# Optimization experiments

Measured on AMD Instinct MI355X. Metric: run time of the kernel, lower is better.

Reference implementation:

```python
import jax, jax.numpy as jnp
import numpy as np

B, S, E, H = 8, 2048, 1024, 64

def setup_inputs() -> dict:
    key = jax.random.key(0)
    k1, k2, k3, k4 = jax.random.split(key, 4)
    scale = 0.02
    return {
        "x": jax.random.normal(k1, (B, S, E), dtype=jnp.float32),
        "Wq": jax.random.normal(k2, (E, H), dtype=jnp.float32) * scale,
        "Wk": jax.random.normal(k3, (E, H), dtype=jnp.float32) * scale,
        "Wv": jax.random.normal(k4, (E, H), dtype=jnp.float32) * scale,
    }

def reference(x, Wq, Wk, Wv):
    # x: [B, S, E]; projections to [B, S, H]
    q = jnp.einsum("bse,eh->bsh", x, Wq)
    k = jnp.einsum("bse,eh->bsh", x, Wk)
    v = jnp.einsum("bse,eh->bsh", x, Wv)
    head_size = Wq.shape[1]
    # NOTE: original divides by head_size (not sqrt(head_size))
    scores = jnp.einsum("bqh,bkh->bqk", q, k) / head_size  # [B, S, S]
    seq = q.shape[1]
    causal = jnp.tril(jnp.ones((seq, seq), dtype=bool))
    scores = jnp.where(causal, scores, -jnp.inf)
    attn = jax.nn.softmax(scores, axis=-1)
    # dropout p=0.0 (eval) -> identity
    return jnp.einsum("bqk,bkh->bqh", attn, v)
```

## Files before the change

kernel.cpp:

```cpp
#include <hip/hip_runtime.h>


typedef __bf16 bf16;
typedef bf16 bf16x8 __attribute__((ext_vector_type(8)));
typedef bf16 bf16x4 __attribute__((ext_vector_type(4)));
typedef float v4f __attribute__((ext_vector_type(4)));

#define MFMA_BF16 __builtin_amdgcn_mfma_f32_16x16x32_bf16

constexpr int SEQ = 2048, EDIM = 1024, HDIM = 64;
constexpr float SCALE_L2E = 1.4426950408889634f / 64.0f;

__global__ __launch_bounds__(256) void prep_w_kernel(
    const float* __restrict__ Wq, const float* __restrict__ Wk,
    const float* __restrict__ Wv, bf16* __restrict__ Wt) {
  int mat = blockIdx.x >> 5, kseg = blockIdx.x & 31;
  const float* src = mat == 0 ? Wq : (mat == 1 ? Wk : Wv);
  int n = threadIdx.x & 63;
  int k0 = kseg * 32 + (threadIdx.x >> 6) * 8;
  bf16x8 v;
#pragma unroll
  for (int j = 0; j < 8; ++j)
    v[j] = (bf16)src[(k0 + j) * 64 + n];
  *reinterpret_cast<bf16x8*>(Wt + (size_t)(mat * 64 + n) * EDIM + k0) = v;
}

__global__ __launch_bounds__(256) void proj_kernel(
    const float* __restrict__ x, const bf16* __restrict__ Wt,
    bf16* __restrict__ qw, bf16* __restrict__ kw, bf16* __restrict__ vT) {
  __shared__ __align__(16) bf16 As[2][32][72];
  __shared__ __align__(16) bf16 Bs[2][192][72];

  const int t = threadIdx.x;
  const int m0 = blockIdx.x * 32;
  const int wv = t >> 6, lane = t & 63, quad = lane >> 4, l16 = lane & 15;

  v4f acc[2][3] = {};
  float4 aReg[2];
  bf16x8 bReg[6];

  auto loadA = [&](int kk) {
#pragma unroll
    for (int p = 0; p < 2; ++p) {
      int flat = p * 1024 + t * 4;
      int r = flat >> 6, c = flat & 63;
      aReg[p] = *reinterpret_cast<const float4*>(
          x + (size_t)(m0 + r) * EDIM + kk * 64 + c);
    }
  };
  auto loadB = [&](int kk) {
#pragma unroll
    for (int p = 0; p < 6; ++p) {
      int idx = p * 256 + t;
      int r = idx >> 3, off = (idx & 7) * 8;
      bReg[p] = *reinterpret_cast<const bf16x8*>(
          Wt + (size_t)r * EDIM + kk * 64 + off);
    }
  };

  loadA(0);
  loadB(0);

  for (int kk = 0; kk < 16; ++kk) {
    const int buf = kk & 1;
#pragma unroll
    for (int p = 0; p < 2; ++p) {
      int flat = p * 1024 + t * 4;
      int r = flat >> 6, c = flat & 63;
      bf16x4 h4 = {(bf16)aReg[p].x, (bf16)aReg[p].y,
                   (bf16)aReg[p].z, (bf16)aReg[p].w};
      *reinterpret_cast<bf16x4*>(&As[buf][r][c]) = h4;
    }
#pragma unroll
    for (int p = 0; p < 6; ++p) {
      int idx = p * 256 + t;
      int r = idx >> 3, off = (idx & 7) * 8;
      *reinterpret_cast<bf16x8*>(&Bs[buf][r][off]) = bReg[p];
    }
    __syncthreads();
    if (kk < 15) {
      loadA(kk + 1);
      loadB(kk + 1);
    }
#pragma unroll
    for (int ks = 0; ks < 2; ++ks) {
      bf16x8 af[2], bfr[3];
#pragma unroll
      for (int mi = 0; mi < 2; ++mi)
        af[mi] = *reinterpret_cast<const bf16x8*>(
            &As[buf][16 * mi + l16][32 * ks + 8 * quad]);
#pragma unroll
      for (int ni = 0; ni < 3; ++ni)
        bfr[ni] = *reinterpret_cast<const bf16x8*>(
            &Bs[buf][48 * wv + 16 * ni + l16][32 * ks + 8 * quad]);
#pragma unroll
      for (int mi = 0; mi < 2; ++mi)
#pragma unroll
        for (int ni = 0; ni < 3; ++ni)
          acc[mi][ni] = MFMA_BF16(af[mi], bfr[ni], acc[mi][ni], 0, 0, 0);
    }
  }

#pragma unroll
  for (int mi = 0; mi < 2; ++mi) {
    const int token0 = m0 + 16 * mi + 4 * quad;
#pragma unroll
    for (int ni = 0; ni < 3; ++ni) {
      int n = 48 * wv + 16 * ni + l16;
      if (n < 64) {
#pragma unroll
        for (int r = 0; r < 4; ++r)
          qw[(size_t)(token0 + r) * HDIM + n] = (bf16)acc[mi][ni][r];
      } else if (n < 128) {
#pragma unroll
        for (int r = 0; r < 4; ++r)
          kw[(size_t)(token0 + r) * HDIM + (n - 64)] = (bf16)acc[mi][ni][r];
      } else {
        int b = token0 >> 11, s0 = token0 & 2047;
        bf16x4 pk = {(bf16)acc[mi][ni][0], (bf16)acc[mi][ni][1],
                     (bf16)acc[mi][ni][2], (bf16)acc[mi][ni][3]};
        *reinterpret_cast<bf16x4*>(
            vT + ((size_t)(b * 64 + (n - 128))) * SEQ + s0) = pk;
      }
    }
  }
}

__global__ __launch_bounds__(512) void attn_kernel(
    const bf16* __restrict__ qw, const bf16* __restrict__ kw,
    const bf16* __restrict__ vT, float* __restrict__ out) {
  const int batch = blockIdx.x & 7;
  const int pi = blockIdx.x >> 3;
  const int w = threadIdx.x >> 6;
  const int lane = threadIdx.x & 63;
  const int quad = lane >> 4, l16 = lane & 15;

  __shared__ __align__(16) bf16 p_lds[8][2][32][68];
  __shared__ __align__(16) float o_lds[8][32][68];
  __shared__ float l_lds[8][32];

  const bf16* qB = qw + (size_t)batch * SEQ * HDIM;
  const bf16* kB = kw + (size_t)batch * SEQ * HDIM;
  const bf16* vB = vT + (size_t)batch * HDIM * SEQ;

  for (int sp = 0; sp < 2; ++sp) {
    const int j = sp ? (63 - pi) : pi;
    const int q0 = 32 * j;
    const int T64 = (j + 2) >> 1;
    const int nw = (T64 > w) ? (((T64 - 1 - w) >> 3) + 1) : 0;

    bf16x8 aq[2][2];
#pragma unroll
    for (int mi = 0; mi < 2; ++mi)
#pragma unroll
      for (int kf = 0; kf < 2; ++kf)
        aq[mi][kf] = *reinterpret_cast<const bf16x8*>(
            qB + (size_t)(q0 + 16 * mi + l16) * HDIM + 32 * kf + 8 * quad);

    v4f accO[2][4] = {};
    float l_part[2][4] = {{0.f, 0.f, 0.f, 0.f}, {0.f, 0.f, 0.f, 0.f}};
    bf16x8 kfr[4][2];

    auto loadK = [&](int jt) {
#pragma unroll
      for (int nt = 0; nt < 4; ++nt)
#pragma unroll
        for (int kf = 0; kf < 2; ++kf)
          kfr[nt][kf] = *reinterpret_cast<const bf16x8*>(
              kB + (size_t)(64 * jt + 16 * nt + l16) * HDIM + 32 * kf +
              8 * quad);
    };
    auto qk_exp_stage = [&](int jt, int slot) {
      v4f s[2][4] = {};
#pragma unroll
      for (int mi = 0; mi < 2; ++mi)
#pragma unroll
        for (int nt = 0; nt < 4; ++nt) {
          s[mi][nt] = MFMA_BF16(aq[mi][0], kfr[nt][0], s[mi][nt], 0, 0, 0);
          s[mi][nt] = MFMA_BF16(aq[mi][1], kfr[nt][1], s[mi][nt], 0, 0, 0);
        }
      const bool last = (jt == T64 - 1);
#pragma unroll
      for (int mi = 0; mi < 2; ++mi)
#pragma unroll
        for (int nt = 0; nt < 4; ++nt)
#pragma unroll
          for (int r = 0; r < 4; ++r) {
            float p = __builtin_amdgcn_exp2f(s[mi][nt][r] * SCALE_L2E);
            if (last &&
                (64 * jt + 16 * nt + l16 > q0 + 16 * mi + 4 * quad + r))
              p = 0.f;
            l_part[mi][r] += p;
            p_lds[w][slot][16 * mi + 4 * quad + r][16 * nt + l16] = (bf16)p;
          }
    };

    if (nw > 0) {
      loadK(w);
      qk_exp_stage(w, 0);
    }
    for (int i = 0; i < nw; ++i) {
      const int jt = w + 8 * i;
      const int k0 = 64 * jt;
      if (i + 1 < nw) loadK(jt + 8);
      bf16x8 vfr[4][2];
#pragma unroll
      for (int nt = 0; nt < 4; ++nt)
#pragma unroll
        for (int kc = 0; kc < 2; ++kc)
          vfr[nt][kc] = *reinterpret_cast<const bf16x8*>(
              vB + (size_t)(16 * nt + l16) * SEQ + k0 + 32 * kc + 8 * quad);
      asm volatile("s_waitcnt lgkmcnt(0)" ::: "memory");
      bf16x8 pa[2][2];
#pragma unroll
      for (int mi = 0; mi < 2; ++mi)
#pragma unroll
        for (int kc = 0; kc < 2; ++kc)
          pa[mi][kc] = *reinterpret_cast<const bf16x8*>(
              &p_lds[w][i & 1][16 * mi + l16][32 * kc + 8 * quad]);
      if (i + 1 < nw) qk_exp_stage(jt + 8, (i + 1) & 1);
#pragma unroll
      for (int mi = 0; mi < 2; ++mi)
#pragma unroll
        for (int nt = 0; nt < 4; ++nt) {
          accO[mi][nt] = MFMA_BF16(pa[mi][0], vfr[nt][0], accO[mi][nt], 0, 0, 0);
          accO[mi][nt] = MFMA_BF16(pa[mi][1], vfr[nt][1], accO[mi][nt], 0, 0, 0);
        }
    }

#pragma unroll
    for (int mi = 0; mi < 2; ++mi)
#pragma unroll
      for (int r = 0; r < 4; ++r) {
        float s = l_part[mi][r];
        s += __shfl_xor(s, 1, 16);
        s += __shfl_xor(s, 2, 16);
        s += __shfl_xor(s, 4, 16);
        s += __shfl_xor(s, 8, 16);
        l_part[mi][r] = s;
      }

    __syncthreads();
#pragma unroll
    for (int mi = 0; mi < 2; ++mi)
#pragma unroll
      for (int nt = 0; nt < 4; ++nt)
#pragma unroll
        for (int r = 0; r < 4; ++r)
          o_lds[w][16 * mi + 4 * quad + r][16 * nt + l16] = accO[mi][nt][r];
    if (l16 == 0) {
#pragma unroll
      for (int mi = 0; mi < 2; ++mi)
#pragma unroll
        for (int r = 0; r < 4; ++r)
          l_lds[w][16 * mi + 4 * quad + r] = l_part[mi][r];
    }
    __syncthreads();

    {
      const int col = threadIdx.x & 63;
      const int r0 = (threadIdx.x >> 6) * 4;
#pragma unroll
      for (int k = 0; k < 4; ++k) {
        const int row = r0 + k;
        float lt = 0.f, s = 0.f;
#pragma unroll
        for (int c = 0; c < 8; ++c) {
          lt += l_lds[c][row];
          s += o_lds[c][row][col];
        }
        out[((size_t)batch * SEQ + q0 + row) * HDIM + col] = s / lt;
      }
    }
  }
}

extern "C" void kernel_launch(void* const* d_in, const int* in_sizes, int n_in,
                              void* d_out, int out_size, void* d_ws,
                              size_t ws_size, hipStream_t stream) {
  const float* x = (const float*)d_in[0];
  const float* Wq = (const float*)d_in[1];
  const float* Wk = (const float*)d_in[2];
  const float* Wv = (const float*)d_in[3];

  char* ws = (char*)d_ws;
  bf16* Wt = (bf16*)(ws);
  bf16* qw = (bf16*)(ws + 0x60000);
  bf16* kw = (bf16*)(ws + 0x260000);
  bf16* vT = (bf16*)(ws + 0x460000);

  prep_w_kernel<<<96, 256, 0, stream>>>(Wq, Wk, Wv, Wt);
  proj_kernel<<<512, 256, 0, stream>>>(x, Wt, qw, kw, vT);
  attn_kernel<<<256, 512, 0, stream>>>(qw, kw, vT, (float*)d_out);
}
```

Measured before the change: 136.7 us.

## Fuse weight prep, projection and attention into one cooperative kernel

```diff
diff --git a/kernel.cpp b/kernel.cpp
--- a/kernel.cpp
+++ b/kernel.cpp
@@ -1,4 +1,7 @@
 #include <hip/hip_runtime.h>
+#include <hip/hip_cooperative_groups.h>
+
+namespace cg = cooperative_groups;
 
 
 typedef __bf16 bf16;
@@ -10,6 +13,286 @@
 
 constexpr int SEQ = 2048, EDIM = 1024, HDIM = 64;
 constexpr float SCALE_L2E = 1.4426950408889634f / 64.0f;
+
+__global__ __launch_bounds__(512, 2) void fused_kernel(
+    const float* __restrict__ x, const float* __restrict__ Wq,
+    const float* __restrict__ Wk, const float* __restrict__ Wv,
+    bf16* __restrict__ Wt, bf16* __restrict__ qw, bf16* __restrict__ kw,
+    bf16* __restrict__ vT, float* __restrict__ out) {
+  __shared__ __align__(16) char smem[140288];
+  const int t = threadIdx.x;
+  const int lane = t & 63;
+  const int quad = lane >> 4, l16 = lane & 15;
+
+  {
+    const int gid = blockIdx.x * 512 + t;
+    if (gid < 24576) {
+      const int n = gid & 63;
+      const int k0 = ((gid >> 6) & 127) * 8;
+      const int mat = gid >> 13;
+      const float* src = mat == 0 ? Wq : (mat == 1 ? Wk : Wv);
+      bf16x8 v;
+#pragma unroll
+      for (int j = 0; j < 8; ++j)
+        v[j] = (bf16)src[(k0 + j) * 64 + n];
+      *reinterpret_cast<bf16x8*>(Wt + (size_t)(mat * 64 + n) * EDIM + k0) = v;
+    }
+  }
+  cg::this_grid().sync();
+
+  {
+    typedef bf16 AsArr[2][64][72];
+    typedef bf16 BsArr[2][192][72];
+    AsArr& As = *reinterpret_cast<AsArr*>(smem);
+    BsArr& Bs = *reinterpret_cast<BsArr*>(smem + sizeof(AsArr));
+
+    const int m0 = blockIdx.x * 64;
+    const int w8 = t >> 6;
+    const int wm = w8 >> 2;
+    const int wn = w8 & 3;
+
+    v4f acc[2][3] = {};
+    float4 aReg[2];
+    bf16x8 bReg[3];
+
+    auto loadA = [&](int kk) {
+#pragma unroll
+      for (int p = 0; p < 2; ++p) {
+        int flat = p * 2048 + t * 4;
+        int r = flat >> 6, c = flat & 63;
+        aReg[p] = *reinterpret_cast<const float4*>(
+            x + (size_t)(m0 + r) * EDIM + kk * 64 + c);
+      }
+    };
+    auto loadB = [&](int kk) {
+#pragma unroll
+      for (int p = 0; p < 3; ++p) {
+        int idx = p * 512 + t;
+        int r = idx >> 3, off = (idx & 7) * 8;
+        bReg[p] = *reinterpret_cast<const bf16x8*>(
+            Wt + (size_t)r * EDIM + kk * 64 + off);
+      }
+    };
+
+    loadA(0);
+    loadB(0);
+
+    for (int kk = 0; kk < 16; ++kk) {
+      const int buf = kk & 1;
+#pragma unroll
+      for (int p = 0; p < 2; ++p) {
+        int flat = p * 2048 + t * 4;
+        int r = flat >> 6, c = flat & 63;
+        bf16x4 h4 = {(bf16)aReg[p].x, (bf16)aReg[p].y,
+                     (bf16)aReg[p].z, (bf16)aReg[p].w};
+        *reinterpret_cast<bf16x4*>(&As[buf][r][c]) = h4;
+      }
+#pragma unroll
+      for (int p = 0; p < 3; ++p) {
+        int idx = p * 512 + t;
+        int r = idx >> 3, off = (idx & 7) * 8;
+        *reinterpret_cast<bf16x8*>(&Bs[buf][r][off]) = bReg[p];
+      }
+      __syncthreads();
+      if (kk < 15) {
+        loadA(kk + 1);
+        loadB(kk + 1);
+      }
+#pragma unroll
+      for (int ks = 0; ks < 2; ++ks) {
+        bf16x8 af[2], bfr[3];
+#pragma unroll
+        for (int mi = 0; mi < 2; ++mi)
+          af[mi] = *reinterpret_cast<const bf16x8*>(
+              &As[buf][32 * wm + 16 * mi + l16][32 * ks + 8 * quad]);
+#pragma unroll
+        for (int ni = 0; ni < 3; ++ni)
+          bfr[ni] = *reinterpret_cast<const bf16x8*>(
+              &Bs[buf][48 * wn + 16 * ni + l16][32 * ks + 8 * quad]);
+#pragma unroll
+        for (int mi = 0; mi < 2; ++mi)
+#pragma unroll
+          for (int ni = 0; ni < 3; ++ni)
+            acc[mi][ni] = MFMA_BF16(af[mi], bfr[ni], acc[mi][ni], 0, 0, 0);
+      }
+    }
+
+#pragma unroll
+    for (int mi = 0; mi < 2; ++mi) {
+      const int token0 = m0 + 32 * wm + 16 * mi + 4 * quad;
+#pragma unroll
+      for (int ni = 0; ni < 3; ++ni) {
+        int n = 48 * wn + 16 * ni + l16;
+        if (n < 64) {
+#pragma unroll
+          for (int r = 0; r < 4; ++r)
+            qw[(size_t)(token0 + r) * HDIM + n] = (bf16)acc[mi][ni][r];
+        } else if (n < 128) {
+#pragma unroll
+          for (int r = 0; r < 4; ++r)
+            kw[(size_t)(token0 + r) * HDIM + (n - 64)] = (bf16)acc[mi][ni][r];
+        } else {
+          int b = token0 >> 11, s0 = token0 & 2047;
+          bf16x4 pk = {(bf16)acc[mi][ni][0], (bf16)acc[mi][ni][1],
+                       (bf16)acc[mi][ni][2], (bf16)acc[mi][ni][3]};
+          *reinterpret_cast<bf16x4*>(
+              vT + ((size_t)(b * 64 + (n - 128))) * SEQ + s0) = pk;
+        }
+      }
+    }
+  }
+  cg::this_grid().sync();
+
+  {
+    typedef bf16 PArr[8][2][32][68];
+    typedef float OArr[8][32][68];
+    typedef float LArr[8][32];
+    PArr& p_lds = *reinterpret_cast<PArr*>(smem);
+    OArr& o_lds = *reinterpret_cast<OArr*>(smem + sizeof(PArr));
+    LArr& l_lds = *reinterpret_cast<LArr*>(smem + sizeof(PArr) + sizeof(OArr));
+
+    const int batch = blockIdx.x & 7;
+    const int pi = blockIdx.x >> 3;
+    const int w = t >> 6;
+
+    const bf16* qB = qw + (size_t)batch * SEQ * HDIM;
+    const bf16* kB = kw + (size_t)batch * SEQ * HDIM;
+    const bf16* vB = vT + (size_t)batch * HDIM * SEQ;
+
+    for (int sp = 0; sp < 2; ++sp) {
+      const int j = sp ? (63 - pi) : pi;
+      const int q0 = 32 * j;
+      const int T64 = (j + 2) >> 1;
+      const int nw = (T64 > w) ? (((T64 - 1 - w) >> 3) + 1) : 0;
+
+      bf16x8 aq[2][2];
+#pragma unroll
+      for (int mi = 0; mi < 2; ++mi)
+#pragma unroll
+        for (int kf = 0; kf < 2; ++kf)
+          aq[mi][kf] = *reinterpret_cast<const bf16x8*>(
+              qB + (size_t)(q0 + 16 * mi + l16) * HDIM + 32 * kf + 8 * quad);
+
+      v4f accO[2][4] = {};
+      float l_part[2][4] = {{0.f, 0.f, 0.f, 0.f}, {0.f, 0.f, 0.f, 0.f}};
+      bf16x8 kfr[4][2];
+
+      auto loadK = [&](int jt) {
+#pragma unroll
+        for (int nt = 0; nt < 4; ++nt)
+#pragma unroll
+          for (int kf = 0; kf < 2; ++kf)
+            kfr[nt][kf] = *reinterpret_cast<const bf16x8*>(
+                kB + (size_t)(64 * jt + 16 * nt + l16) * HDIM + 32 * kf +
+                8 * quad);
+      };
+      auto qk_exp_stage = [&](int jt, int slot) {
+        v4f s[2][4] = {};
+#pragma unroll
+        for (int mi = 0; mi < 2; ++mi)
+#pragma unroll
+          for (int nt = 0; nt < 4; ++nt) {
+            s[mi][nt] = MFMA_BF16(aq[mi][0], kfr[nt][0], s[mi][nt], 0, 0, 0);
+            s[mi][nt] = MFMA_BF16(aq[mi][1], kfr[nt][1], s[mi][nt], 0, 0, 0);
+          }
+        const bool last = (jt == T64 - 1);
+#pragma unroll
+        for (int mi = 0; mi < 2; ++mi)
+#pragma unroll
+          for (int nt = 0; nt < 4; ++nt)
+#pragma unroll
+            for (int r = 0; r < 4; ++r) {
+              float p = __builtin_amdgcn_exp2f(s[mi][nt][r] * SCALE_L2E);
+              if (last &&
+                  (64 * jt + 16 * nt + l16 > q0 + 16 * mi + 4 * quad + r))
+                p = 0.f;
+              l_part[mi][r] += p;
+              p_lds[w][slot][16 * mi + 4 * quad + r][16 * nt + l16] = (bf16)p;
+            }
+      };
+
+      if (nw > 0) {
+        loadK(w);
+        qk_exp_stage(w, 0);
+      }
+      for (int i = 0; i < nw; ++i) {
+        const int jt = w + 8 * i;
+        const int k0 = 64 * jt;
+        if (i + 1 < nw) loadK(jt + 8);
+        bf16x8 vfr[4][2];
+#pragma unroll
+        for (int nt = 0; nt < 4; ++nt)
+#pragma unroll
+          for (int kc = 0; kc < 2; ++kc)
+            vfr[nt][kc] = *reinterpret_cast<const bf16x8*>(
+                vB + (size_t)(16 * nt + l16) * SEQ + k0 + 32 * kc + 8 * quad);
+        asm volatile("s_waitcnt lgkmcnt(0)" ::: "memory");
+        bf16x8 pa[2][2];
+#pragma unroll
+        for (int mi = 0; mi < 2; ++mi)
+#pragma unroll
+          for (int kc = 0; kc < 2; ++kc)
+            pa[mi][kc] = *reinterpret_cast<const bf16x8*>(
+                &p_lds[w][i & 1][16 * mi + l16][32 * kc + 8 * quad]);
+        if (i + 1 < nw) qk_exp_stage(jt + 8, (i + 1) & 1);
+#pragma unroll
+        for (int mi = 0; mi < 2; ++mi)
+#pragma unroll
+          for (int nt = 0; nt < 4; ++nt) {
+            accO[mi][nt] =
+                MFMA_BF16(pa[mi][0], vfr[nt][0], accO[mi][nt], 0, 0, 0);
+            accO[mi][nt] =
+                MFMA_BF16(pa[mi][1], vfr[nt][1], accO[mi][nt], 0, 0, 0);
+          }
+      }
+
+#pragma unroll
+      for (int mi = 0; mi < 2; ++mi)
+#pragma unroll
+        for (int r = 0; r < 4; ++r) {
+          float s = l_part[mi][r];
+          s += __shfl_xor(s, 1, 16);
+          s += __shfl_xor(s, 2, 16);
+          s += __shfl_xor(s, 4, 16);
+          s += __shfl_xor(s, 8, 16);
+          l_part[mi][r] = s;
+        }
+
+      __syncthreads();
+#pragma unroll
+      for (int mi = 0; mi < 2; ++mi)
+#pragma unroll
+        for (int nt = 0; nt < 4; ++nt)
+#pragma unroll
+          for (int r = 0; r < 4; ++r)
+            o_lds[w][16 * mi + 4 * quad + r][16 * nt + l16] = accO[mi][nt][r];
+      if (l16 == 0) {
+#pragma unroll
+        for (int mi = 0; mi < 2; ++mi)
+#pragma unroll
+          for (int r = 0; r < 4; ++r)
+            l_lds[w][16 * mi + 4 * quad + r] = l_part[mi][r];
+      }
+      __syncthreads();
+
+      {
+        const int col = t & 63;
+        const int r0 = (t >> 6) * 4;
+#pragma unroll
+        for (int k = 0; k < 4; ++k) {
+          const int row = r0 + k;
+          float lt = 0.f, s = 0.f;
+#pragma unroll
+          for (int c = 0; c < 8; ++c) {
+            lt += l_lds[c][row];
+            s += o_lds[c][row][col];
+          }
+          out[((size_t)batch * SEQ + q0 + row) * HDIM + col] = s / lt;
+        }
+      }
+    }
+  }
+}
 
 __global__ __launch_bounds__(256) void prep_w_kernel(
     const float* __restrict__ Wq, const float* __restrict__ Wk,
@@ -288,8 +571,15 @@
   bf16* qw = (bf16*)(ws + 0x60000);
   bf16* kw = (bf16*)(ws + 0x260000);
   bf16* vT = (bf16*)(ws + 0x460000);
-
-  prep_w_kernel<<<96, 256, 0, stream>>>(Wq, Wk, Wv, Wt);
-  proj_kernel<<<512, 256, 0, stream>>>(x, Wt, qw, kw, vT);
-  attn_kernel<<<256, 512, 0, stream>>>(qw, kw, vT, (float*)d_out);
+  float* out = (float*)d_out;
+
+  void* args[] = {(void*)&x,  (void*)&Wq, (void*)&Wk, (void*)&Wv, (void*)&Wt,
+                  (void*)&qw, (void*)&kw, (void*)&vT, (void*)&out};
+  hipError_t err = hipLaunchCooperativeKernel(
+      (const void*)fused_kernel, dim3(256), dim3(512), args, 0, stream);
+  if (err != hipSuccess) {
+    prep_w_kernel<<<96, 256, 0, stream>>>(Wq, Wk, Wv, Wt);
+    proj_kernel<<<512, 256, 0, stream>>>(x, Wt, qw, kw, vT);
+    attn_kernel<<<256, 512, 0, stream>>>(qw, kw, vT, (float*)d_out);
+  }
 }
```

Measured after the change: 208.3 us. 1.52x slower.
